# Kernel tuning notes

Measured on AMD Instinct MI355X. Metric: run time of the kernel, lower is better.

Reference implementation:

```python
import jax, jax.numpy as jnp
import numpy as np
from jax import lax

B, V, C, H, W = 2, 8, 64, 128, 128
A = 256
C3 = 3 * C + 2  # 194 input channels for refine/confidence branches
CO = 3 * C      # 192 output channels of branch_refine
GROUPS = 8      # _group_count(192, 8) == 8
HID = max(4, CO // 4)  # 48 hidden channels in ChannelGate2d


def _conv3(x, w, b):
    y = lax.conv_general_dilated(x, w, (1, 1), 'SAME',
                                 dimension_numbers=('NCHW', 'OIHW', 'NCHW'))
    return y + b[None, :, None, None]


def _group_norm(x, scale, bias, groups, eps=1e-5):
    b, c, h, w = x.shape
    xg = x.reshape(b, groups, c // groups, h, w)
    mu = xg.mean(axis=(2, 3, 4), keepdims=True)
    var = xg.var(axis=(2, 3, 4), keepdims=True)
    xn = ((xg - mu) / jnp.sqrt(var + eps)).reshape(b, c, h, w)
    return xn * scale[None, :, None, None] + bias[None, :, None, None]


def _channel_gate(x, w1, b1, w2, b2):
    pooled = x.mean(axis=(2, 3))                     # [B,C]
    h = jax.nn.silu(pooled @ w1.T + b1)              # [B,HID]
    gate = jax.nn.sigmoid(h @ w2.T + b2)             # [B,C]
    return x * (0.5 + gate)[:, :, None, None]


def _conv_block(x, p):
    h = jax.nn.silu(_group_norm(_conv3(x, p['c1w'], p['c1b']), p['g1s'], p['g1b'], GROUPS))
    h = jax.nn.silu(_group_norm(_conv3(h, p['c2w'], p['c2b']), p['g2s'], p['g2b'], GROUPS))
    h = _channel_gate(h, p['gw1'], p['gb1'], p['gw2'], p['gb2'])
    res = jnp.einsum('bchw,oc->bohw', x, p['rpw']) + p['rpb'][None, :, None, None]
    return h + jnp.tanh(p['rs']) * res


def _fuse(vf, uvs, masks, importance, atlas_size):
    # vf:[B,V,C,H,W] uvs:[B,V,H,W,2] masks:[B,V,1,H,W] importance:[B,V]
    b, v, c, h, w = vf.shape
    P = atlas_size * atlas_size
    weights = jnp.maximum(importance.astype(vf.dtype), 0.0)
    finite = jnp.isfinite(uvs).all(axis=-1)                 # [B,V,H,W]
    valid = (masks[:, :, 0] > 0.5) & finite & (weights[:, :, None, None] > 0.0)
    safe = jnp.where(finite[..., None], uvs, 0.0)
    xi = jnp.round(jnp.clip(safe[..., 0], 0.0, 1.0) * (atlas_size - 1)).astype(jnp.int32)
    yi = jnp.round((1.0 - jnp.clip(safe[..., 1], 0.0, 1.0)) * (atlas_size - 1)).astype(jnp.int32)
    idx = (yi * atlas_size + xi).reshape(b, v * h * w)      # [B,N]
    wvalid = valid.astype(vf.dtype) * weights[:, :, None, None]
    feat = (vf * wvalid[:, :, None]).transpose(0, 2, 1, 3, 4).reshape(b, c, v * h * w)
    cnt = wvalid.reshape(b, v * h * w)

    def per_sample(f, cc, i):
        atlas = jax.ops.segment_sum(f.T, i, num_segments=P).T   # [C,P]
        counts = jax.ops.segment_sum(cc, i, num_segments=P)     # [P]
        return atlas, counts

    atlas, counts = jax.vmap(per_sample)(feat, cnt, idx)
    atlas = atlas.reshape(b, c, atlas_size, atlas_size)
    counts = counts.reshape(b, 1, atlas_size, atlas_size)
    fused = atlas / jnp.maximum(counts, 1.0)
    return fused, (counts > 0).astype(vf.dtype)


def _normalize_per_sample(t, eps=1e-6):
    scale = jnp.maximum(t.reshape(t.shape[0], -1).max(axis=1), eps)
    return jnp.clip(t / scale[:, None, None, None], 0.0, 1.0)


def setup_inputs() -> dict:
    key = jax.random.key(0)
    ks = jax.random.split(key, 20)
    inp = {
        'encoded_views': jax.random.normal(ks[0], (B, V, C, H, W), jnp.float32),
        'view_uvs': jax.random.uniform(ks[1], (B, V, H, W, 2), jnp.float32),
        'view_masks': jax.random.uniform(ks[2], (B, V, 1, H, W), jnp.float32),
        'w_global': jax.random.uniform(ks[3], (B, V), jnp.float32),
        'w_boundary': jax.random.uniform(ks[4], (B, V), jnp.float32),
        'w_highlight': jax.random.uniform(ks[5], (B, V), jnp.float32),
        'atlas_size': A,
        # ConvBlock params (random instead of zero-init so all paths are exercised)
        'c1w': jax.random.normal(ks[6], (CO, C3, 3, 3), jnp.float32) * 0.02,
        'c1b': jnp.zeros((CO,), jnp.float32),
        'g1s': jnp.ones((CO,), jnp.float32),
        'g1b': jnp.zeros((CO,), jnp.float32),
        'c2w': jax.random.normal(ks[7], (CO, CO, 3, 3), jnp.float32) * 0.02,
        'c2b': jnp.zeros((CO,), jnp.float32),
        'g2s': jnp.ones((CO,), jnp.float32),
        'g2b': jnp.zeros((CO,), jnp.float32),
        'gw1': jax.random.normal(ks[8], (HID, CO), jnp.float32) * 0.05,
        'gb1': jnp.zeros((HID,), jnp.float32),
        'gw2': jax.random.normal(ks[9], (CO, HID), jnp.float32) * 0.05,
        'gb2': jnp.zeros((CO,), jnp.float32),
        'rpw': jax.random.normal(ks[10], (CO, C3), jnp.float32) * 0.05,
        'rpb': jnp.zeros((CO,), jnp.float32),
        'rs': jnp.array(0.3, jnp.float32),
        'conf_w': jax.random.normal(ks[11], (3, C3), jnp.float32) * 0.05,
        'conf_b': jnp.zeros((3,), jnp.float32),
        'mix_scale': jnp.array(0.5, jnp.float32),
    }
    return inp


def reference(encoded_views, view_uvs, view_masks, w_global, w_boundary, w_highlight,
              atlas_size, c1w, c1b, g1s, g1b, c2w, c2b, g2s, g2b,
              gw1, gb1, gw2, gb2, rpw, rpb, rs, conf_w, conf_b, mix_scale):
    p = dict(c1w=c1w, c1b=c1b, g1s=g1s, g1b=g1b, c2w=c2w, c2b=c2b, g2s=g2s, g2b=g2b,
             gw1=gw1, gb1=gb1, gw2=gw2, gb2=gb2, rpw=rpw, rpb=rpb, rs=rs)
    g_feat, g_val = _fuse(encoded_views, view_uvs, view_masks, w_global, atlas_size)
    b_feat, b_val = _fuse(encoded_views, view_uvs, view_masks, w_boundary, atlas_size)
    h_feat, h_val = _fuse(encoded_views, view_uvs, view_masks, w_highlight, atlas_size)
    coverage = jnp.clip((g_val + b_val + h_val) / 3.0, 0.0, 1.0)
    stack = jnp.stack([g_feat, b_feat, h_feat], axis=1)     # [B,3,C,A,A]
    uncertainty = jnp.sqrt(stack.var(axis=1).mean(axis=1, keepdims=True))
    uncertainty = _normalize_per_sample(uncertainty) * coverage
    ctx = jnp.concatenate([g_feat, b_feat, h_feat, coverage, uncertainty], axis=1)
    refine = _conv_block(ctx, p)
    rg, rb, rh = jnp.split(refine, 3, axis=1)
    conf = jax.nn.sigmoid(jnp.einsum('bchw,oc->bohw', ctx, conf_w) + conf_b[None, :, None, None])
    ms = jnp.tanh(mix_scale)
    g_out = g_feat + ms * rg * conf[:, 0:1]
    b_out = b_feat + ms * rb * conf[:, 1:2]
    h_out = h_feat + ms * rh * conf[:, 2:3]
    return (g_out, b_out, h_out, coverage, uncertainty, conf)
```

## Files before the change

kernel.cpp:

```cpp
#include <hip/hip_runtime.h>
#include <math.h>

#define B_ 2
#define V_ 8
#define C_ 64
#define HW_ 16384
#define A_ 256
#define P_ 65536
#define CO_ 192
#define CPG_ 24
#define NG_ 8
#define ICP1 224
#define ICP2 192

#define OFF_ACC   0ull
#define SZ_ACC    (2ull*65536*192*4)
#define OFF_CNT   (OFF_ACC + SZ_ACC)
#define SZ_CNT    (2ull*3*65536*4)
#define OFF_CTXB  (OFF_CNT + SZ_CNT)
#define SZ_CTXB   (2ull*65536*224*2)
#define OFF_H1A   (OFF_CTXB + SZ_CTXB)
#define SZ_H1A    (2ull*65536*192*2)
#define OFF_W1    (OFF_H1A + SZ_H1A)
#define SZ_W1     (9ull*192*224*2)
#define OFF_W2    (OFF_W1 + SZ_W1)
#define SZ_W2     (9ull*192*192*2)
#define OFF_SM    (OFF_W2 + SZ_W2 + 256)

#define SM_STATS1 0
#define SM_STATS2 256
#define SM_SCALE  512
#define SM_POOLED 1024
#define SM_GATE   2560
#define SM_RAWU   8192

#define OUT_B    8388608
#define OUT_COV  25165824
#define OUT_UNC  25296896
#define OUT_CONF 25427968

typedef __attribute__((ext_vector_type(4))) float f32x4;
typedef __attribute__((ext_vector_type(8))) short bf16x8;

__device__ __forceinline__ float sigmoidf_(float x){ return 1.f/(1.f+expf(-x)); }
__device__ __forceinline__ float bf2f(unsigned short h){ return __uint_as_float(((unsigned)h)<<16); }
__device__ __forceinline__ unsigned short f2bf(float f){
  unsigned u = __float_as_uint(f);
  return (unsigned short)((u + 0x7fffu + ((u>>16)&1u)) >> 16);
}

__global__ __launch_bounds__(256) void k_prep(const float* __restrict__ c1w,
    const float* __restrict__ c2w, unsigned short* __restrict__ w1p, unsigned short* __restrict__ w2p)
{
  int idx = blockIdx.x*256 + threadIdx.x;
  const int N1 = 9*192*224;
  if (idx < N1){
    int ic = idx % 224; int oc = (idx/224) % 192; int k = idx/(224*192);
    float v = (ic < 194) ? c1w[(size_t)(oc*194+ic)*9 + k] : 0.f;
    w1p[idx] = f2bf(v);
  } else {
    int i2 = idx - N1;
    if (i2 < 9*192*192){
      int ic = i2 % 192; int oc = (i2/192) % 192; int k = i2/(192*192);
      w2p[i2] = f2bf(c2w[(size_t)(oc*192+ic)*9 + k]);
    }
  }
}

__global__ __launch_bounds__(256) void k_fuse(const float* __restrict__ vf,
    const float* __restrict__ uvs, const float* __restrict__ masks,
    const float* __restrict__ wgp, const float* __restrict__ wbp, const float* __restrict__ whp,
    float* __restrict__ acc, float* __restrict__ cnt)
{
  __shared__ __align__(16) float sf[64*65];
  __shared__ int sidx[64];
  __shared__ int svalid[64];
  __shared__ float sw[3];
  int t = threadIdx.x;
  int pix0 = blockIdx.x*64;
  int b   = pix0 / (V_*HW_);
  int rem = pix0 % (V_*HW_);
  int v   = rem / HW_;
  int p2  = rem % HW_;
  size_t vbase = ((size_t)(b*V_+v))*C_*HW_;
  for (int i=0;i<16;i++){
    int f = t + i*256;
    int c = f>>6, px = f&63;
    sf[c*65+px] = vf[vbase + (size_t)c*HW_ + p2 + px];
  }
  if (t<64){
    const float* u2 = uvs + (((size_t)(b*V_+v))*HW_ + p2 + t)*2;
    float ux = u2[0], uy = u2[1];
    int fin = isfinite(ux) && isfinite(uy);
    float su = fin?ux:0.f, svv = fin?uy:0.f;
    float cu = fminf(fmaxf(su,0.f),1.f);
    float cv = fminf(fmaxf(svv,0.f),1.f);
    int xi = (int)rintf(cu*255.f);
    int yi = (int)rintf((1.f-cv)*255.f);
    sidx[t] = yi*256+xi;
    float m = masks[((size_t)(b*V_+v))*HW_ + p2 + t];
    svalid[t] = (m>0.5f) && fin;
  }
  if (t<3){
    const float* wp = (t==0)?wgp:((t==1)?wbp:whp);
    sw[t] = fmaxf(wp[b*V_+v], 0.f);
  }
  __syncthreads();
  int wave = t>>6, lane = t&63;
  float w0 = sw[0], w1 = sw[1], w2 = sw[2];
  for (int i=0;i<16;i++){
    int px = wave*16+i;
    if (!svalid[px]) continue;
    int bin = sidx[px];
    float val = sf[lane*65+px];
    size_t base = ((size_t)b*P_ + bin)*192;
    if (w0>0.f) atomicAdd(&acc[base + lane],        val*w0);
    if (w1>0.f) atomicAdd(&acc[base + 64 + lane],   val*w1);
    if (w2>0.f) atomicAdd(&acc[base + 128 + lane],  val*w2);
    if (lane<3){
      float wv = sw[lane];
      if (wv>0.f) atomicAdd(&cnt[((size_t)(b*3+lane))*P_ + bin], wv);
    }
  }
}

__global__ __launch_bounds__(256) void k_finalize(const float* __restrict__ acc,
      const float* __restrict__ cnt, unsigned short* __restrict__ ctxb,
      float* __restrict__ out_cov, float* __restrict__ raw_unc, int* __restrict__ scale)
{
  __shared__ __align__(16) float sv[64*193];
  __shared__ float sc[3][64];
  __shared__ float up[256];
  __shared__ float s_cov[64];
  __shared__ float s_unc[64];
  int t = threadIdx.x;
  int bin0 = blockIdx.x*64;
  int b = bin0 >> 16;
  int p0 = bin0 & 65535;
  size_t abase = ((size_t)b*P_ + p0)*192;
  for (int i=0;i<48;i++){
    int f = t + i*256;
    int bl = f/192, c = f - bl*192;
    sv[bl*193+c] = acc[abase + f];
  }
  if (t<192){
    int br = t>>6, bl = t&63;
    sc[br][bl] = cnt[((size_t)(b*3+br))*P_ + p0 + bl];
  }
  __syncthreads();
  {
    int bl = t>>2, q = t&3;
    float dg = 1.f/fmaxf(sc[0][bl],1.f);
    float db = 1.f/fmaxf(sc[1][bl],1.f);
    float dh = 1.f/fmaxf(sc[2][bl],1.f);
    float s = 0.f;
    for (int j=0;j<16;j++){
      int c = q*16+j;
      float fg = sv[bl*193+c]*dg;
      float fb = sv[bl*193+64+c]*db;
      float fh = sv[bl*193+128+c]*dh;
      sv[bl*193+c]=fg; sv[bl*193+64+c]=fb; sv[bl*193+128+c]=fh;
      float m = (fg+fb+fh)*(1.f/3.f);
      float d0=fg-m, d1=fb-m, d2=fh-m;
      s += d0*d0+d1*d1+d2*d2;
    }
    up[t] = s;
  }
  __syncthreads();
  if (t<64){
    float tot = up[t*4]+up[t*4+1]+up[t*4+2]+up[t*4+3];
    float u = sqrtf(tot*(1.f/192.f));
    float vg = sc[0][t]>0.f?1.f:0.f;
    float vb = sc[1][t]>0.f?1.f:0.f;
    float vh = sc[2][t]>0.f?1.f:0.f;
    float cov = fminf(fmaxf((vg+vb+vh)*(1.f/3.f),0.f),1.f);
    s_cov[t] = cov; s_unc[t] = u;
    out_cov[(size_t)b*P_ + p0 + t] = cov;
    raw_unc[(size_t)b*P_ + p0 + t] = u;
    atomicMax(&scale[b], __float_as_int(u));
  }
  __syncthreads();
  for (int f=t; f<1792; f+=256){
    int cg = f % 28, bl = f / 28;
    int c0 = cg*8;
    unsigned short h[8];
    #pragma unroll
    for (int j=0;j<8;j++){
      int c = c0+j;
      float vv;
      if (c < 192)      vv = sv[bl*193+c];
      else if (c==192)  vv = s_cov[bl];
      else if (c==193)  vv = s_unc[bl];
      else              vv = 0.f;
      h[j] = f2bf(vv);
    }
    *(uint4*)&ctxb[((size_t)b*P_ + p0 + bl)*ICP1 + c0] = *(uint4*)h;
  }
}

__global__ __launch_bounds__(256) void k_norm_unc(unsigned short* __restrict__ ctxb,
    const int* __restrict__ scale, const float* __restrict__ raw_unc,
    const float* __restrict__ out_cov, float* __restrict__ out_unc)
{
  int tid = blockIdx.x*256 + threadIdx.x;
  int b = tid >> 16;
  float s = fmaxf(__int_as_float(scale[b]), 1e-6f);
  float u = raw_unc[tid];
  float cov = out_cov[tid];
  float un = fminf(fmaxf(u/s,0.f),1.f)*cov;
  out_unc[tid] = un;
  ctxb[(size_t)tid*ICP1 + 193] = f2bf(un);
}

template<int ICP, int CHUNKS>
__global__ __launch_bounds__(256,4) void k_conv3(const unsigned short* __restrict__ X,
    const unsigned short* __restrict__ Wp, const float* __restrict__ bias, float* __restrict__ Y)
{
  __shared__ short s_in[258*32];
  __shared__ short s_w[192*32];
  int t = threadIdx.x;
  int y0 = blockIdx.x;
  int oc0 = blockIdx.y*64;
  int b = blockIdx.z;
  int wv = t>>6, lane = t&63, l15 = lane&15, quad = lane>>4;
  f32x4 acc[4][4];
  #pragma unroll
  for (int mt=0;mt<4;mt++){
    float4 bv = *(const float4*)&bias[oc0 + mt*16 + quad*4];
    f32x4 iv; iv.x=bv.x; iv.y=bv.y; iv.z=bv.z; iv.w=bv.w;
    #pragma unroll
    for (int nt=0;nt<4;nt++) acc[mt][nt]=iv;
  }
  const unsigned short* Xb = X + (size_t)b*P_*ICP;
  for (int ch=0; ch<CHUNKS; ++ch){
    int ic0 = ch*32;
    for (int ky=0; ky<3; ky++){
      int gy = y0 + ky - 1;
      if ((unsigned)gy >= 256u) continue;
      __syncthreads();
      for (int f=t; f<1032; f+=256){
        int icq = f&3, xi = f>>2;
        int gx = xi - 1;
        uint4 vval = make_uint4(0,0,0,0);
        if ((unsigned)gx < 256u)
          vval = *(const uint4*)&Xb[(size_t)(gy*256+gx)*ICP + ic0 + icq*8];
        *(uint4*)&s_in[xi*32 + ((icq ^ ((xi>>1)&3)))*8] = vval;
      }
      for (int f=t; f<768; f+=256){
        int icq = f&3, oc = (f>>2)&63, kx = f>>8;
        uint4 vval = *(const uint4*)&Wp[(size_t)((ky*3+kx)*192 + oc0 + oc)*ICP + ic0 + icq*8];
        int r = kx*64 + oc;
        *(uint4*)&s_w[r*32 + ((icq ^ ((r>>1)&3)))*8] = vval;
      }
      __syncthreads();
      #pragma unroll
      for (int kx=0;kx<3;kx++){
        bf16x8 Af[4], Bf[4];
        #pragma unroll
        for (int mt=0;mt<4;mt++){
          int r = kx*64 + mt*16 + l15;
          Af[mt] = *(const bf16x8*)&s_w[r*32 + (((quad ^ ((r>>1)&3)))&3)*8];
        }
        #pragma unroll
        for (int nt=0;nt<4;nt++){
          int r = wv*64 + nt*16 + l15 + kx;
          Bf[nt] = *(const bf16x8*)&s_in[r*32 + (((quad ^ ((r>>1)&3)))&3)*8];
        }
        #pragma unroll
        for (int mt=0;mt<4;mt++)
          #pragma unroll
          for (int nt=0;nt<4;nt++)
            acc[mt][nt] = __builtin_amdgcn_mfma_f32_16x16x32_bf16(Af[mt], Bf[nt], acc[mt][nt], 0, 0, 0);
      }
    }
  }
  float* Yb = Y + (size_t)b*P_*192;
  #pragma unroll
  for (int mt=0;mt<4;mt++){
    int oc = oc0 + mt*16 + quad*4;
    #pragma unroll
    for (int nt=0;nt<4;nt++){
      int px = wv*64 + nt*16 + l15;
      *(f32x4*)&Yb[(size_t)(y0*256+px)*192 + oc] = acc[mt][nt];
    }
  }
}

__global__ __launch_bounds__(256) void k_gn_stats(const float* __restrict__ x, double* __restrict__ stats)
{
  int b = blockIdx.y; int y0 = blockIdx.x*2;
  const float* base = x + ((size_t)b*P_ + y0*256)*192;
  int t = threadIdx.x;
  double s1[3]={0,0,0}, s2[3]={0,0,0};
  for (int j=0;j<96;j++){
    int f4 = t + j*256;
    float4 v = *(const float4*)&base[(size_t)f4*4];
    int r = j - (j/3)*3;
    s1[r] += (double)v.x + (double)v.y + (double)v.z + (double)v.w;
    s2[r] += (double)v.x*v.x + (double)v.y*v.y + (double)v.z*v.z + (double)v.w*v.w;
  }
  __shared__ double red[16];
  if (t<16) red[t]=0.0;
  __syncthreads();
  #pragma unroll
  for (int r=0;r<3;r++){
    int c = (4*t + 64*r) % 192;
    int g = c/24;
    atomicAdd(&red[g*2],   s1[r]);
    atomicAdd(&red[g*2+1], s2[r]);
  }
  __syncthreads();
  if (t<8){
    atomicAdd(&stats[(b*8+t)*2],   red[t*2]);
    atomicAdd(&stats[(b*8+t)*2+1], red[t*2+1]);
  }
}

__global__ __launch_bounds__(256) void k_gn1_apply(const float* __restrict__ x, const double* __restrict__ stats,
    const float* __restrict__ gs, const float* __restrict__ gb, unsigned short* __restrict__ y)
{
  size_t i8 = ((size_t)blockIdx.x*256 + threadIdx.x)*8;
  int b = (int)(i8 / ((size_t)192*P_));
  int c = (int)(i8 % 192);
  int bg = b*8 + c/24;
  const double N = 24.0*65536.0;
  double mu = stats[bg*2]/N;
  double var = stats[bg*2+1]/N - mu*mu;
  float rstd = 1.0f/sqrtf((float)var + 1e-5f);
  float mean = (float)mu;
  float4 sA = *(const float4*)&gs[c];
  float4 sB = *(const float4*)&gs[c+4];
  float4 bA = *(const float4*)&gb[c];
  float4 bB = *(const float4*)&gb[c+4];
  float4 v0 = *(const float4*)&x[i8];
  float4 v1 = *(const float4*)&x[i8+4];
  float xin[8] = {v0.x,v0.y,v0.z,v0.w,v1.x,v1.y,v1.z,v1.w};
  float scl[8] = {sA.x,sA.y,sA.z,sA.w,sB.x,sB.y,sB.z,sB.w};
  float bia[8] = {bA.x,bA.y,bA.z,bA.w,bB.x,bB.y,bB.z,bB.w};
  unsigned short h[8];
  #pragma unroll
  for (int i=0;i<8;i++){
    float xn = (xin[i]-mean)*rstd*scl[i] + bia[i];
    h[i] = f2bf(xn*sigmoidf_(xn));
  }
  *(uint4*)&y[i8] = *(uint4*)h;
}

__global__ __launch_bounds__(256) void k_gn2_apply(float* __restrict__ x, const double* __restrict__ stats,
    const float* __restrict__ gs, const float* __restrict__ gb)
{
  size_t i8 = ((size_t)blockIdx.x*256 + threadIdx.x)*8;
  int b = (int)(i8 / ((size_t)192*P_));
  int c = (int)(i8 % 192);
  int bg = b*8 + c/24;
  const double N = 24.0*65536.0;
  double mu = stats[bg*2]/N;
  double var = stats[bg*2+1]/N - mu*mu;
  float rstd = 1.0f/sqrtf((float)var + 1e-5f);
  float mean = (float)mu;
  float4 sA = *(const float4*)&gs[c];
  float4 sB = *(const float4*)&gs[c+4];
  float4 bA = *(const float4*)&gb[c];
  float4 bB = *(const float4*)&gb[c+4];
  float4 v0 = *(const float4*)&x[i8];
  float4 v1 = *(const float4*)&x[i8+4];
  float xin[8] = {v0.x,v0.y,v0.z,v0.w,v1.x,v1.y,v1.z,v1.w};
  float scl[8] = {sA.x,sA.y,sA.z,sA.w,sB.x,sB.y,sB.z,sB.w};
  float bia[8] = {bA.x,bA.y,bA.z,bA.w,bB.x,bB.y,bB.z,bB.w};
  #pragma unroll
  for (int i=0;i<8;i++){
    float xn = (xin[i]-mean)*rstd*scl[i] + bia[i];
    xin[i] = xn*sigmoidf_(xn);
  }
  *(float4*)&x[i8]   = make_float4(xin[0],xin[1],xin[2],xin[3]);
  *(float4*)&x[i8+4] = make_float4(xin[4],xin[5],xin[6],xin[7]);
}

__global__ __launch_bounds__(256) void k_pool(const float* __restrict__ x, float* __restrict__ pooled)
{
  int b = blockIdx.y; int y0 = blockIdx.x*4;
  const float* base = x + ((size_t)b*P_ + y0*256)*192;
  int t = threadIdx.x;
  float4 p[3];
  #pragma unroll
  for (int r=0;r<3;r++) p[r] = make_float4(0.f,0.f,0.f,0.f);
  for (int j=0;j<192;j++){
    int f4 = t + j*256;
    float4 v = *(const float4*)&base[(size_t)f4*4];
    int r = j - (j/3)*3;
    p[r].x += v.x; p[r].y += v.y; p[r].z += v.z; p[r].w += v.w;
  }
  __shared__ float pl[192];
  if (t<192) pl[t]=0.f;
  __syncthreads();
  #pragma unroll
  for (int r=0;r<3;r++){
    int c = (4*t + 64*r) % 192;
    atomicAdd(&pl[c],   p[r].x);
    atomicAdd(&pl[c+1], p[r].y);
    atomicAdd(&pl[c+2], p[r].z);
    atomicAdd(&pl[c+3], p[r].w);
  }
  __syncthreads();
  if (t<192) atomicAdd(&pooled[b*192+t], pl[t]*(1.f/65536.f));
}

__global__ void k_gate(const float* __restrict__ pooled, const float* __restrict__ gw1,
    const float* __restrict__ gb1, const float* __restrict__ gw2, const float* __restrict__ gb2,
    float* __restrict__ gatef)
{
  __shared__ float hb[2*48];
  int t = threadIdx.x;
  if (t<96){
    int b=t/48, j=t%48;
    float a = gb1[j];
    for (int c=0;c<192;c++) a = fmaf(pooled[b*192+c], gw1[j*192+c], a);
    hb[t] = a*sigmoidf_(a);
  }
  __syncthreads();
  for (int i=t;i<384;i+=256){
    int b=i/192, c=i%192;
    float a = gb2[c];
    for (int j=0;j<48;j++) a = fmaf(hb[b*48+j], gw2[c*48+j], a);
    gatef[i] = 0.5f + sigmoidf_(a);
  }
}

__global__ __launch_bounds__(256) void k_conf(const unsigned short* __restrict__ ctxb,
    const float* __restrict__ cw, const float* __restrict__ cbias, float* __restrict__ out_conf)
{
  __shared__ float scw[3*224];
  int t = threadIdx.x;
  for (int f=t; f<672; f+=256){
    int c = f % 224, o = f / 224;
    scw[f] = (c<194) ? cw[o*194 + c] : 0.f;
  }
  __syncthreads();
  int tid = blockIdx.x*256 + t;
  int b = tid >> 16, p = tid & 65535;
  const unsigned short* cp = ctxb + ((size_t)b*P_ + p)*ICP1;
  float a0 = cbias[0], a1 = cbias[1], a2 = cbias[2];
  for (int q=0;q<28;q++){
    uint4 v = *(const uint4*)&cp[q*8];
    unsigned wd[4] = {v.x,v.y,v.z,v.w};
    #pragma unroll
    for (int j=0;j<8;j++){
      unsigned bits = wd[j>>1];
      float xf = (j&1) ? __uint_as_float(bits & 0xffff0000u) : __uint_as_float(bits<<16);
      int c = q*8+j;
      a0 = fmaf(xf, scw[c],       a0);
      a1 = fmaf(xf, scw[224+c],   a1);
      a2 = fmaf(xf, scw[448+c],   a2);
    }
  }
  out_conf[((size_t)(b*3+0))*P_ + p] = sigmoidf_(a0);
  out_conf[((size_t)(b*3+1))*P_ + p] = sigmoidf_(a1);
  out_conf[((size_t)(b*3+2))*P_ + p] = sigmoidf_(a2);
}

__global__ __launch_bounds__(256,4) void k_combine(const unsigned short* __restrict__ ctxb,
    const float* __restrict__ h2, const float* __restrict__ rpw, const float* __restrict__ rpb,
    const float* __restrict__ gatef, const float* __restrict__ conf_out,
    const float* __restrict__ rs, const float* __restrict__ mix, float* __restrict__ dout)
{
  __shared__ short s_x[256*32];
  __shared__ short s_w[64*32];
  int t = threadIdx.x;
  size_t p0 = (size_t)blockIdx.x*256;
  int oc0 = blockIdx.y*64, br = blockIdx.y;
  int wv = t>>6, lane = t&63, l15 = lane&15, quad = lane>>4;
  f32x4 acc[4][4];
  #pragma unroll
  for (int mt=0;mt<4;mt++){
    float4 bv = *(const float4*)&rpb[oc0 + mt*16 + quad*4];
    f32x4 iv; iv.x=bv.x; iv.y=bv.y; iv.z=bv.z; iv.w=bv.w;
    #pragma unroll
    for (int nt=0;nt<4;nt++) acc[mt][nt]=iv;
  }
  for (int ch=0; ch<7; ch++){
    int ic0 = ch*32;
    __syncthreads();
    for (int f=t; f<1024; f+=256){
      int icq = f&3, px = f>>2;
      uint4 v = *(const uint4*)&ctxb[(p0+px)*ICP1 + ic0 + icq*8];
      *(uint4*)&s_x[px*32 + ((icq ^ ((px>>1)&3)))*8] = v;
    }
    {
      int oc = t&63, icq = t>>6;
      unsigned short h[8];
      #pragma unroll
      for (int j=0;j<8;j++){
        int ic = ic0 + icq*8 + j;
        h[j] = (ic<194) ? f2bf(rpw[(size_t)(oc0+oc)*194 + ic]) : (unsigned short)0;
      }
      *(uint4*)&s_w[oc*32 + ((icq ^ ((oc>>1)&3)))*8] = *(uint4*)h;
    }
    __syncthreads();
    bf16x8 Af[4], Bf[4];
    #pragma unroll
    for (int mt=0;mt<4;mt++){
      int r = mt*16 + l15;
      Af[mt] = *(const bf16x8*)&s_w[r*32 + (((quad ^ ((r>>1)&3)))&3)*8];
    }
    #pragma unroll
    for (int nt=0;nt<4;nt++){
      int r = wv*64 + nt*16 + l15;
      Bf[nt] = *(const bf16x8*)&s_x[r*32 + (((quad ^ ((r>>1)&3)))&3)*8];
    }
    #pragma unroll
    for (int mt=0;mt<4;mt++)
      #pragma unroll
      for (int nt=0;nt<4;nt++)
        acc[mt][nt] = __builtin_amdgcn_mfma_f32_16x16x32_bf16(Af[mt], Bf[nt], acc[mt][nt], 0, 0, 0);
  }
  float trs = tanhf(rs[0]);
  float ms2 = tanhf(mix[0]);
  int b = (int)(p0 >> 16);
  #pragma unroll
  for (int mt=0;mt<4;mt++){
    int oc = oc0 + mt*16 + quad*4;
    int cc = oc & 63;
    float4 gv = *(const float4*)&gatef[b*192 + oc];
    #pragma unroll
    for (int nt=0;nt<4;nt++){
      size_t pf = p0 + wv*64 + nt*16 + l15;
      int p = (int)(pf & 65535);
      ushort4 fh = *(const ushort4*)&ctxb[pf*ICP1 + oc];
      float4 hv = *(const float4*)&h2[pf*192 + oc];
      float cf = conf_out[((size_t)(b*3+br))*P_ + p];
      size_t dst = (size_t)br*OUT_B + ((size_t)(b*64+cc))*P_ + p;
      dout[dst]            = bf2f(fh.x) + ms2*(hv.x*gv.x + trs*acc[mt][nt].x)*cf;
      dout[dst + P_]       = bf2f(fh.y) + ms2*(hv.y*gv.y + trs*acc[mt][nt].y)*cf;
      dout[dst + 2*P_]     = bf2f(fh.z) + ms2*(hv.z*gv.z + trs*acc[mt][nt].z)*cf;
      dout[dst + 3*P_]     = bf2f(fh.w) + ms2*(hv.w*gv.w + trs*acc[mt][nt].w)*cf;
    }
  }
}

extern "C" void kernel_launch(void* const* d_in, const int* in_sizes, int n_in,
                              void* d_out, int out_size, void* d_ws, size_t ws_size,
                              hipStream_t stream)
{
  const float* vf    = (const float*)d_in[0];
  const float* uvs   = (const float*)d_in[1];
  const float* masks = (const float*)d_in[2];
  const float* wg    = (const float*)d_in[3];
  const float* wb    = (const float*)d_in[4];
  const float* wh    = (const float*)d_in[5];
  const float* c1w = (const float*)d_in[7];
  const float* c1b = (const float*)d_in[8];
  const float* g1s = (const float*)d_in[9];
  const float* g1b = (const float*)d_in[10];
  const float* c2w = (const float*)d_in[11];
  const float* c2b = (const float*)d_in[12];
  const float* g2s = (const float*)d_in[13];
  const float* g2b = (const float*)d_in[14];
  const float* gw1 = (const float*)d_in[15];
  const float* gb1 = (const float*)d_in[16];
  const float* gw2 = (const float*)d_in[17];
  const float* gb2 = (const float*)d_in[18];
  const float* rpw = (const float*)d_in[19];
  const float* rpb = (const float*)d_in[20];
  const float* rs  = (const float*)d_in[21];
  const float* cw  = (const float*)d_in[22];
  const float* cb  = (const float*)d_in[23];
  const float* mix = (const float*)d_in[24];

  char* ws = (char*)d_ws;
  float*          accb  = (float*)(ws + OFF_ACC);
  float*          cntb  = (float*)(ws + OFF_CNT);
  unsigned short* ctxb  = (unsigned short*)(ws + OFF_CTXB);
  unsigned short* h1act = (unsigned short*)(ws + OFF_H1A);
  unsigned short* w1p   = (unsigned short*)(ws + OFF_W1);
  unsigned short* w2p   = (unsigned short*)(ws + OFF_W2);
  float*  h1raw  = (float*)(ws + OFF_ACC);
  float*  h2     = (float*)(ws + OFF_ACC);
  double* stats1 = (double*)(ws + OFF_SM + SM_STATS1);
  double* stats2 = (double*)(ws + OFF_SM + SM_STATS2);
  int*    scale  = (int*)(ws + OFF_SM + SM_SCALE);
  float*  pooled = (float*)(ws + OFF_SM + SM_POOLED);
  float*  gatef  = (float*)(ws + OFF_SM + SM_GATE);
  float*  rawu   = (float*)(ws + OFF_SM + SM_RAWU);

  float* out = (float*)d_out;
  float* out_cov  = out + OUT_COV;
  float* out_unc  = out + OUT_UNC;
  float* out_conf = out + OUT_CONF;

  hipMemsetAsync(ws + OFF_ACC, 0, SZ_ACC + SZ_CNT, stream);
  hipMemsetAsync(ws + OFF_SM, 0, 8192, stream);

  k_prep<<<2808, 256, 0, stream>>>(c1w, c2w, w1p, w2p);
  k_fuse<<<4096, 256, 0, stream>>>(vf, uvs, masks, wg, wb, wh, accb, cntb);
  k_finalize<<<2048, 256, 0, stream>>>(accb, cntb, ctxb, out_cov, rawu, scale);
  k_norm_unc<<<512, 256, 0, stream>>>(ctxb, scale, rawu, out_cov, out_unc);
  k_conv3<ICP1,7><<<dim3(256,3,2), 256, 0, stream>>>(ctxb, w1p, c1b, h1raw);
  k_gn_stats<<<dim3(128,2), 256, 0, stream>>>(h1raw, stats1);
  k_gn1_apply<<<12288, 256, 0, stream>>>(h1raw, stats1, g1s, g1b, h1act);
  k_conv3<ICP2,6><<<dim3(256,3,2), 256, 0, stream>>>(h1act, w2p, c2b, h2);
  k_gn_stats<<<dim3(128,2), 256, 0, stream>>>(h2, stats2);
  k_gn2_apply<<<12288, 256, 0, stream>>>(h2, stats2, g2s, g2b);
  k_pool<<<dim3(64,2), 256, 0, stream>>>(h2, pooled);
  k_gate<<<1, 256, 0, stream>>>(pooled, gw1, gb1, gw2, gb2, gatef);
  k_conf<<<512, 256, 0, stream>>>(ctxb, cw, cb, out_conf);
  k_combine<<<dim3(512,3), 256, 0, stream>>>(ctxb, h2, rpw, rpb, gatef, out_conf, rs, mix, out);
}
```

Measured before the change: 860.0 us.

## Double-buffer conv with direct-to-LDS loads and fuse GN stats and pooling

The 3x3 conv kernels now stage input rows and weights into double-buffered LDS using global_load_lds, so the next tile's load overlaps MFMA work. Blocks are remapped so neighbouring rows land on the same XCD, and launch bounds drop to 2 waves per SIMD to fit the larger LDS footprint. GroupNorm statistics are reduced from the accumulators in the conv epilogue, which removes the separate k_gn_stats passes over the fp32 activations. The GN2 apply kernel also accumulates the channel pooling, which removes k_pool. The trade-offs are lower occupancy, float rather than double partial sums for the statistics, and reliance on vmcnt and barrier ordering for correctness.

```diff
diff --git a/kernel.cpp b/kernel.cpp
--- a/kernel.cpp
+++ b/kernel.cpp
@@ -47,6 +47,11 @@
 __device__ __forceinline__ unsigned short f2bf(float f){
   unsigned u = __float_as_uint(f);
   return (unsigned short)((u + 0x7fffu + ((u>>16)&1u)) >> 16);
+}
+
+__device__ __forceinline__ void gl_lds16(const void* g, void* l){
+  __builtin_amdgcn_global_load_lds((const __attribute__((address_space(1))) void*)g,
+                                   (__attribute__((address_space(3))) void*)l, 16, 0, 0);
 }
 
 __global__ __launch_bounds__(256) void k_prep(const float* __restrict__ c1w,
@@ -213,16 +218,23 @@
 }
 
 template<int ICP, int CHUNKS>
-__global__ __launch_bounds__(256,4) void k_conv3(const unsigned short* __restrict__ X,
-    const unsigned short* __restrict__ Wp, const float* __restrict__ bias, float* __restrict__ Y)
-{
-  __shared__ short s_in[258*32];
-  __shared__ short s_w[192*32];
+__global__ __launch_bounds__(256,2) void k_conv3(const unsigned short* __restrict__ X,
+    const unsigned short* __restrict__ Wp, const float* __restrict__ bias, float* __restrict__ Y,
+    double* __restrict__ stats)
+{
+  __shared__ short s_in[2][258*32];
+  __shared__ short s_w[2][192*32];
+  __shared__ float sred[2][64];
+  __shared__ float gsm[16];
   int t = threadIdx.x;
-  int y0 = blockIdx.x;
-  int oc0 = blockIdx.y*64;
-  int b = blockIdx.z;
+  int f_ = blockIdx.x + 256*(blockIdx.y + 3*blockIdx.z);
+  int xcd = f_ & 7; int g_ = f_ >> 3;
+  int y0  = xcd*32 + (g_ & 31);
+  int h_  = g_ >> 5;
+  int b   = h_ & 1;
+  int oc0 = (h_ >> 1)*64;
   int wv = t>>6, lane = t&63, l15 = lane&15, quad = lane>>4;
+
   f32x4 acc[4][4];
   #pragma unroll
   for (int mt=0;mt<4;mt++){
@@ -231,40 +243,68 @@
     #pragma unroll
     for (int nt=0;nt<4;nt++) acc[mt][nt]=iv;
   }
+
   const unsigned short* Xb = X + (size_t)b*P_*ICP;
-  for (int ch=0; ch<CHUNKS; ++ch){
+  int kyLo = (y0==0)?1:0;
+  int kyHi = (y0==255)?1:2;
+  int nky  = kyHi - kyLo + 1;
+  int NP   = CHUNKS*nky;
+
+  if (t < 128){
+    int bufi = t>>6, j = t&63;
+    int idx = (j<32) ? j : (257*32 + (j-32));
+    s_in[bufi][idx] = 0;
+  }
+  if (t < 128) sred[t>>6][t&63] = 0.f;
+  if (t < 16)  gsm[t] = 0.f;
+
+  auto stage = [&](int p, int bufi){
+    int ch = p / nky; int ky = kyLo + (p - ch*nky);
     int ic0 = ch*32;
-    for (int ky=0; ky<3; ky++){
-      int gy = y0 + ky - 1;
-      if ((unsigned)gy >= 256u) continue;
-      __syncthreads();
-      for (int f=t; f<1032; f+=256){
-        int icq = f&3, xi = f>>2;
-        int gx = xi - 1;
-        uint4 vval = make_uint4(0,0,0,0);
-        if ((unsigned)gx < 256u)
-          vval = *(const uint4*)&Xb[(size_t)(gy*256+gx)*ICP + ic0 + icq*8];
-        *(uint4*)&s_in[xi*32 + ((icq ^ ((xi>>1)&3)))*8] = vval;
-      }
-      for (int f=t; f<768; f+=256){
-        int icq = f&3, oc = (f>>2)&63, kx = f>>8;
-        uint4 vval = *(const uint4*)&Wp[(size_t)((ky*3+kx)*192 + oc0 + oc)*ICP + ic0 + icq*8];
-        int r = kx*64 + oc;
-        *(uint4*)&s_w[r*32 + ((icq ^ ((r>>1)&3)))*8] = vval;
-      }
-      __syncthreads();
+    int gy = y0 + ky - 1;
+    const unsigned short* src = Xb + ((size_t)gy*256)*ICP + ic0;
+    #pragma unroll
+    for (int i=0;i<4;i++){
+      int f = t + i*256;
+      int xi = 1 + (f>>2), icq = f&3;
+      int icg = icq ^ ((xi>>1)&3);
+      gl_lds16(src + (size_t)(xi-1)*ICP + icg*8, &s_in[bufi][32 + f*8]);
+    }
+    const unsigned short* wsrc = Wp + ((size_t)(ky*3)*192 + oc0)*ICP + ic0;
+    #pragma unroll
+    for (int i=0;i<3;i++){
+      int f = t + i*256;
+      int kx = f>>8, oc = (f>>2)&63, icq = f&3;
+      int r = kx*64 + oc;
+      int icg = icq ^ ((r>>1)&3);
+      gl_lds16(wsrc + (size_t)(kx*192 + oc)*ICP + icg*8, &s_w[bufi][f*8]);
+    }
+  };
+
+  stage(0, 0);
+  if (NP > 1) stage(1, 1);
+  asm volatile("s_waitcnt lgkmcnt(0)" ::: "memory");
+
+  for (int p=0; p<NP; ++p){
+    if (p+1 < NP) asm volatile("s_waitcnt vmcnt(7)" ::: "memory");
+    else          asm volatile("s_waitcnt vmcnt(0)" ::: "memory");
+    __builtin_amdgcn_s_barrier();
+    __builtin_amdgcn_sched_barrier(0);
+    {
+      const short* si = &s_in[p&1][0];
+      const short* sw = &s_w[p&1][0];
       #pragma unroll
       for (int kx=0;kx<3;kx++){
         bf16x8 Af[4], Bf[4];
         #pragma unroll
         for (int mt=0;mt<4;mt++){
           int r = kx*64 + mt*16 + l15;
-          Af[mt] = *(const bf16x8*)&s_w[r*32 + (((quad ^ ((r>>1)&3)))&3)*8];
+          Af[mt] = *(const bf16x8*)&sw[r*32 + ((quad ^ ((r>>1)&3))&3)*8];
         }
         #pragma unroll
         for (int nt=0;nt<4;nt++){
           int r = wv*64 + nt*16 + l15 + kx;
-          Bf[nt] = *(const bf16x8*)&s_in[r*32 + (((quad ^ ((r>>1)&3)))&3)*8];
+          Bf[nt] = *(const bf16x8*)&si[r*32 + ((quad ^ ((r>>1)&3))&3)*8];
         }
         #pragma unroll
         for (int mt=0;mt<4;mt++)
@@ -273,7 +313,11 @@
             acc[mt][nt] = __builtin_amdgcn_mfma_f32_16x16x32_bf16(Af[mt], Bf[nt], acc[mt][nt], 0, 0, 0);
       }
     }
-  }
+    __builtin_amdgcn_s_barrier();
+    __builtin_amdgcn_sched_barrier(0);
+    if (p+2 < NP) stage(p+2, p&1);
+  }
+
   float* Yb = Y + (size_t)b*P_*192;
   #pragma unroll
   for (int mt=0;mt<4;mt++){
@@ -284,35 +328,35 @@
       *(f32x4*)&Yb[(size_t)(y0*256+px)*192 + oc] = acc[mt][nt];
     }
   }
-}
-
-__global__ __launch_bounds__(256) void k_gn_stats(const float* __restrict__ x, double* __restrict__ stats)
-{
-  int b = blockIdx.y; int y0 = blockIdx.x*2;
-  const float* base = x + ((size_t)b*P_ + y0*256)*192;
-  int t = threadIdx.x;
-  double s1[3]={0,0,0}, s2[3]={0,0,0};
-  for (int j=0;j<96;j++){
-    int f4 = t + j*256;
-    float4 v = *(const float4*)&base[(size_t)f4*4];
-    int r = j - (j/3)*3;
-    s1[r] += (double)v.x + (double)v.y + (double)v.z + (double)v.w;
-    s2[r] += (double)v.x*v.x + (double)v.y*v.y + (double)v.z*v.z + (double)v.w*v.w;
-  }
-  __shared__ double red[16];
-  if (t<16) red[t]=0.0;
-  __syncthreads();
-  #pragma unroll
-  for (int r=0;r<3;r++){
-    int c = (4*t + 64*r) % 192;
-    int g = c/24;
-    atomicAdd(&red[g*2],   s1[r]);
-    atomicAdd(&red[g*2+1], s2[r]);
-  }
-  __syncthreads();
-  if (t<8){
-    atomicAdd(&stats[(b*8+t)*2],   red[t*2]);
-    atomicAdd(&stats[(b*8+t)*2+1], red[t*2+1]);
+
+  #pragma unroll
+  for (int mt=0;mt<4;mt++)
+    #pragma unroll
+    for (int j=0;j<4;j++){
+      float v1 = acc[mt][0][j]+acc[mt][1][j]+acc[mt][2][j]+acc[mt][3][j];
+      float v2 = acc[mt][0][j]*acc[mt][0][j]+acc[mt][1][j]*acc[mt][1][j]
+               + acc[mt][2][j]*acc[mt][2][j]+acc[mt][3][j]*acc[mt][3][j];
+      v1 += __shfl_xor(v1,1); v1 += __shfl_xor(v1,2); v1 += __shfl_xor(v1,4); v1 += __shfl_xor(v1,8);
+      v2 += __shfl_xor(v2,1); v2 += __shfl_xor(v2,2); v2 += __shfl_xor(v2,4); v2 += __shfl_xor(v2,8);
+      if (l15==0){
+        int ocl = mt*16 + quad*4 + j;
+        atomicAdd(&sred[0][ocl], v1);
+        atomicAdd(&sred[1][ocl], v2);
+      }
+    }
+  __syncthreads();
+  if (t < 64){
+    int g = (oc0 + t)/24;
+    atomicAdd(&gsm[g*2],   sred[0][t]);
+    atomicAdd(&gsm[g*2+1], sred[1][t]);
+  }
+  __syncthreads();
+  if (t < 8){
+    int glo = oc0/24, ghi = (oc0+63)/24;
+    if (t >= glo && t <= ghi){
+      atomicAdd(&stats[(b*8+t)*2],   (double)gsm[t*2]);
+      atomicAdd(&stats[(b*8+t)*2+1], (double)gsm[t*2+1]);
+    }
   }
 }
 
@@ -347,62 +391,54 @@
 }
 
 __global__ __launch_bounds__(256) void k_gn2_apply(float* __restrict__ x, const double* __restrict__ stats,
-    const float* __restrict__ gs, const float* __restrict__ gb)
-{
-  size_t i8 = ((size_t)blockIdx.x*256 + threadIdx.x)*8;
-  int b = (int)(i8 / ((size_t)192*P_));
-  int c = (int)(i8 % 192);
-  int bg = b*8 + c/24;
-  const double N = 24.0*65536.0;
-  double mu = stats[bg*2]/N;
-  double var = stats[bg*2+1]/N - mu*mu;
-  float rstd = 1.0f/sqrtf((float)var + 1e-5f);
-  float mean = (float)mu;
+    const float* __restrict__ gs, const float* __restrict__ gb, float* __restrict__ pooled)
+{
+  __shared__ float pl[384];
+  int t = threadIdx.x;
+  for (int f=t; f<384; f+=256) pl[f]=0.f;
+  int tid = blockIdx.x*256 + t;
+  int c = (tid*8) % 192;
   float4 sA = *(const float4*)&gs[c];
   float4 sB = *(const float4*)&gs[c+4];
   float4 bA = *(const float4*)&gb[c];
   float4 bB = *(const float4*)&gb[c+4];
-  float4 v0 = *(const float4*)&x[i8];
-  float4 v1 = *(const float4*)&x[i8+4];
-  float xin[8] = {v0.x,v0.y,v0.z,v0.w,v1.x,v1.y,v1.z,v1.w};
   float scl[8] = {sA.x,sA.y,sA.z,sA.w,sB.x,sB.y,sB.z,sB.w};
   float bia[8] = {bA.x,bA.y,bA.z,bA.w,bB.x,bB.y,bB.z,bB.w};
-  #pragma unroll
-  for (int i=0;i<8;i++){
-    float xn = (xin[i]-mean)*rstd*scl[i] + bia[i];
-    xin[i] = xn*sigmoidf_(xn);
-  }
-  *(float4*)&x[i8]   = make_float4(xin[0],xin[1],xin[2],xin[3]);
-  *(float4*)&x[i8+4] = make_float4(xin[4],xin[5],xin[6],xin[7]);
-}
-
-__global__ __launch_bounds__(256) void k_pool(const float* __restrict__ x, float* __restrict__ pooled)
-{
-  int b = blockIdx.y; int y0 = blockIdx.x*4;
-  const float* base = x + ((size_t)b*P_ + y0*256)*192;
-  int t = threadIdx.x;
-  float4 p[3];
-  #pragma unroll
-  for (int r=0;r<3;r++) p[r] = make_float4(0.f,0.f,0.f,0.f);
-  for (int j=0;j<192;j++){
-    int f4 = t + j*256;
-    float4 v = *(const float4*)&base[(size_t)f4*4];
-    int r = j - (j/3)*3;
-    p[r].x += v.x; p[r].y += v.y; p[r].z += v.z; p[r].w += v.w;
-  }
-  __shared__ float pl[192];
-  if (t<192) pl[t]=0.f;
-  __syncthreads();
-  #pragma unroll
-  for (int r=0;r<3;r++){
-    int c = (4*t + 64*r) % 192;
-    atomicAdd(&pl[c],   p[r].x);
-    atomicAdd(&pl[c+1], p[r].y);
-    atomicAdd(&pl[c+2], p[r].z);
-    atomicAdd(&pl[c+3], p[r].w);
-  }
-  __syncthreads();
-  if (t<192) atomicAdd(&pooled[b*192+t], pl[t]*(1.f/65536.f));
+  float mean[2], rstd[2];
+  #pragma unroll
+  for (int bb=0;bb<2;bb++){
+    int bg = bb*8 + c/24;
+    const double N = 24.0*65536.0;
+    double mu = stats[bg*2]/N;
+    double var = stats[bg*2+1]/N - mu*mu;
+    rstd[bb] = 1.0f/sqrtf((float)var + 1e-5f);
+    mean[bb] = (float)mu;
+  }
+  float pacc[2][8] = {{0.f}};
+  __syncthreads();
+  #pragma unroll
+  for (int k=0;k<8;k++){
+    size_t i8 = ((size_t)tid + (size_t)k*393216)*8;
+    int bb = k>>2;
+    float4 v0 = *(const float4*)&x[i8];
+    float4 v1 = *(const float4*)&x[i8+4];
+    float xin[8] = {v0.x,v0.y,v0.z,v0.w,v1.x,v1.y,v1.z,v1.w};
+    #pragma unroll
+    for (int i=0;i<8;i++){
+      float xn = (xin[i]-mean[bb])*rstd[bb]*scl[i] + bia[i];
+      xn = xn*sigmoidf_(xn);
+      xin[i] = xn;
+      pacc[bb][i] += xn;
+    }
+    *(float4*)&x[i8]   = make_float4(xin[0],xin[1],xin[2],xin[3]);
+    *(float4*)&x[i8+4] = make_float4(xin[4],xin[5],xin[6],xin[7]);
+  }
+  #pragma unroll
+  for (int bb=0;bb<2;bb++)
+    #pragma unroll
+    for (int i=0;i<8;i++) atomicAdd(&pl[bb*192 + c + i], pacc[bb][i]);
+  __syncthreads();
+  for (int f=t; f<384; f+=256) atomicAdd(&pooled[f], pl[f]*(1.f/65536.f));
 }
 
 __global__ void k_gate(const float* __restrict__ pooled, const float* __restrict__ gw1,
@@ -594,13 +630,10 @@
   k_fuse<<<4096, 256, 0, stream>>>(vf, uvs, masks, wg, wb, wh, accb, cntb);
   k_finalize<<<2048, 256, 0, stream>>>(accb, cntb, ctxb, out_cov, rawu, scale);
   k_norm_unc<<<512, 256, 0, stream>>>(ctxb, scale, rawu, out_cov, out_unc);
-  k_conv3<ICP1,7><<<dim3(256,3,2), 256, 0, stream>>>(ctxb, w1p, c1b, h1raw);
-  k_gn_stats<<<dim3(128,2), 256, 0, stream>>>(h1raw, stats1);
+  k_conv3<ICP1,7><<<dim3(256,3,2), 256, 0, stream>>>(ctxb, w1p, c1b, h1raw, stats1);
   k_gn1_apply<<<12288, 256, 0, stream>>>(h1raw, stats1, g1s, g1b, h1act);
-  k_conv3<ICP2,6><<<dim3(256,3,2), 256, 0, stream>>>(h1act, w2p, c2b, h2);
-  k_gn_stats<<<dim3(128,2), 256, 0, stream>>>(h2, stats2);
-  k_gn2_apply<<<12288, 256, 0, stream>>>(h2, stats2, g2s, g2b);
-  k_pool<<<dim3(64,2), 256, 0, stream>>>(h2, pooled);
+  k_conv3<ICP2,6><<<dim3(256,3,2), 256, 0, stream>>>(h1act, w2p, c2b, h2, stats2);
+  k_gn2_apply<<<1536, 256, 0, stream>>>(h2, stats2, g2s, g2b, pooled);
   k_gate<<<1, 256, 0, stream>>>(pooled, gw1, gb1, gw2, gb2, gatef);
   k_conf<<<512, 256, 0, stream>>>(ctxb, cw, cb, out_conf);
   k_combine<<<dim3(512,3), 256, 0, stream>>>(ctxb, h2, rpw, rpb, gatef, out_conf, rs, mix, out);
```

Result: faster. 774.4 us (-9.9%).
